# Kernel optimization log

Hardware: AMD Instinct MI355X
Metric: run time of the kernel (lower is better)

The kernel has to match this reference:

```python
import jax, jax.numpy as jnp
import numpy as np

B, N, L, H, V, OV, MAX_STEPS = 16, 256, 4, 128, 512, 1000, 48


def setup_inputs() -> dict:
    key = jax.random.key(0)
    ks = jax.random.split(key, 20)
    s = lambda fan_in: 1.0 / np.sqrt(fan_in)
    return {
        'data': jax.random.randint(ks[0], (B, N, L), 0, V, dtype=jnp.int32),
        'true_branch_nodes': jax.random.randint(ks[1], (B, N), 0, N, dtype=jnp.int32),
        'false_branch_nodes': jax.random.randint(ks[2], (B, N), 0, N, dtype=jnp.int32),
        'start_index': jax.random.randint(ks[3], (B,), 0, N, dtype=jnp.int32),
        'exit_index': jax.random.randint(ks[4], (B,), 0, N, dtype=jnp.int32),
        'steps': jax.random.randint(ks[5], (B,), 1, MAX_STEPS + 1, dtype=jnp.int32),
        'embed_w': jax.random.uniform(ks[6], (V, H), jnp.float32, -0.1, 0.1),
        'Wi0': jax.random.normal(ks[7], (H, 4 * H), jnp.float32) * s(H),
        'Wh0': jax.random.normal(ks[8], (H, 4 * H), jnp.float32) * s(H),
        'b0': jnp.zeros((4 * H,), jnp.float32),
        'Wi1': jax.random.normal(ks[9], (H, 4 * H), jnp.float32) * s(H),
        'Wh1': jax.random.normal(ks[10], (H, 4 * H), jnp.float32) * s(H),
        'b1': jnp.zeros((4 * H,), jnp.float32),
        'branch_w': jax.random.normal(ks[11], (4 * H, 2), jnp.float32) * s(4 * H),
        'branch_b': jax.random.normal(ks[12], (2,), jnp.float32) * 1e-6,
        'out_w': jax.random.normal(ks[13], (H, OV), jnp.float32) * s(H),
        'out_b': jax.random.normal(ks[14], (OV,), jnp.float32) * 1e-6,
    }


def _lstm(c, h, x, Wi, Wh, b):
    # flax LSTMCell gate order: i, f, g, o
    z = x @ Wi + h @ Wh + b
    i, f, g, o = jnp.split(z, 4, axis=-1)
    c = jax.nn.sigmoid(f) * c + jax.nn.sigmoid(i) * jnp.tanh(g)
    h = jax.nn.sigmoid(o) * jnp.tanh(c)
    return c, h


def reference(data, true_branch_nodes, false_branch_nodes, start_index, exit_index, steps,
              embed_w, Wi0, Wh0, b0, Wi1, Wh1, b1, branch_w, branch_b, out_w, out_b):
    num_nodes = data.shape[1]

    def single_example(data_e, true_idx, false_idx, start, exit_i, n_steps):
        emb_t = jnp.swapaxes(embed_w[data_e], 0, 1)  # [L, N, H]
        hs0 = tuple(jnp.zeros((num_nodes, H), embed_w.dtype) for _ in range(4))  # (c0,h0,c1,h1)
        ip0 = jnp.zeros((num_nodes,), embed_w.dtype).at[start].set(1.0)

        def execute(hs):
            # run 2-layer stacked LSTM over each node's statement tokens (vectorized over nodes)
            def tok_step(carry, x):
                c0, h0, c1, h1 = carry
                c0, h0 = _lstm(c0, h0, x, Wi0, Wh0, b0)
                c1, h1 = _lstm(c1, h1, h0, Wi1, Wh1, b1)
                return (c0, h0, c1, h1), None
            carry, _ = jax.lax.scan(tok_step, hs, emb_t)
            return carry

        def step(carry, idx):
            hs, ip = carry
            contrib = execute(hs)
            # exit node keeps its previous hidden state
            contrib = tuple(c.at[exit_i].set(h[exit_i]) for c, h in zip(contrib, hs))
            concat = jnp.concatenate(contrib, axis=-1)  # [N, 4H]
            p = jax.nn.softmax(concat @ branch_w + branch_b, axis=-1)
            pt, pf = p[:, 0], p[:, 1]
            wt, wf = pt * ip, pf * ip
            ip_new = (jax.ops.segment_sum(wt, true_idx, num_segments=num_nodes)
                      + jax.ops.segment_sum(wf, false_idx, num_segments=num_nodes))
            denom = (ip_new + 1e-7)[:, None]
            def agg(hleaf):
                t = jax.ops.segment_sum(hleaf * wt[:, None], true_idx, num_segments=num_nodes)
                f = jax.ops.segment_sum(hleaf * wf[:, None], false_idx, num_segments=num_nodes)
                return (t + f) / denom
            hs_new = tuple(agg(hleaf) for hleaf in contrib)
            active = idx < n_steps
            hs = tuple(jnp.where(active, new, old) for new, old in zip(hs_new, hs))
            ip = jnp.where(active, ip_new, ip)
            return (hs, ip), None

        (hs, ip), _ = jax.lax.scan(step, (hs0, ip0), jnp.arange(MAX_STEPS))
        return hs[3][exit_i] @ out_w + out_b  # top-layer h at exit node -> [OV]

    return jax.vmap(single_example)(data, true_branch_nodes, false_branch_nodes,
                                    start_index, exit_index, steps)
```

## Files before the change

kernel.cpp:

```cpp
#include <hip/hip_runtime.h>

namespace {
constexpr int B = 16, N = 256, L = 4, H = 128, V = 512, OV = 1000, MAX_STEPS = 48;
constexpr int Z = 4 * H;
constexpr int BN = B * N;
constexpr int PADK = 132;
}

typedef __attribute__((ext_vector_type(8))) short short8;
typedef __attribute__((ext_vector_type(4))) float f32x4;

union F8 {
    short8 s;
    uint4 u;
    uint2 h[2];
};

__device__ __forceinline__ float sigf(float x) { return 1.0f / (1.0f + __expf(-x)); }
__device__ __forceinline__ float tanh_f(float x) { return 1.0f - 2.0f / (__expf(2.0f * x) + 1.0f); }

__device__ __forceinline__ unsigned short bf16_rne(float x) {
    unsigned u = __float_as_uint(x);
    return (unsigned short)((u + 0x7fffu + ((u >> 16) & 1u)) >> 16);
}
__device__ __forceinline__ void split2(float x, unsigned short& hi, unsigned short& lo) {
    hi = bf16_rne(x);
    const float hf = __uint_as_float(((unsigned)hi) << 16);
    lo = bf16_rne(x - hf);
}

__global__ __launch_bounds__(256) void k_init(float4* __restrict__ cur4,
                                              float* __restrict__ ip,
                                              const int* __restrict__ start) {
    const int idx = blockIdx.x * 256 + threadIdx.x;
    cur4[idx] = make_float4(0.f, 0.f, 0.f, 0.f);
    if (idx < BN) ip[idx] = ((idx & (N - 1)) == start[idx >> 8]) ? 1.0f : 0.0f;
}

__global__ __launch_bounds__(256) void k_tokz(const float* __restrict__ emb,
                                              const float* __restrict__ Wi0,
                                              const float* __restrict__ b0,
                                              float* __restrict__ tokz) {
    __shared__ float lds_a[16 * 128];
    float4* l4 = (float4*)lds_a;
    const int tid = threadIdx.x;
    const int c = tid & 127, rg = tid >> 7;
    const int row0 = blockIdx.x * 16;
    {
        const float4* a4 = (const float4*)emb;
        l4[tid] = a4[row0 * 32 + tid];
        l4[tid + 256] = a4[row0 * 32 + tid + 256];
    }
    __syncthreads();
    float acc[8][4];
    {
        float bq[4];
#pragma unroll
        for (int q = 0; q < 4; q++) bq[q] = b0[c + q * 128];
#pragma unroll
        for (int i = 0; i < 8; i++)
#pragma unroll
            for (int q = 0; q < 4; q++) acc[i][q] = bq[q];
    }
    for (int k4 = 0; k4 < 32; k4++) {
        float4 a[8];
#pragma unroll
        for (int i = 0; i < 8; i++) a[i] = l4[(rg * 8 + i) * 32 + k4];
#pragma unroll
        for (int j = 0; j < 4; j++) {
            const int k = k4 * 4 + j;
            const float* wr = Wi0 + k * Z + c;
            const float w0 = wr[0], w1 = wr[128], w2 = wr[256], w3 = wr[384];
#pragma unroll
            for (int i = 0; i < 8; i++) {
                const float av = (j == 0) ? a[i].x : (j == 1) ? a[i].y : (j == 2) ? a[i].z : a[i].w;
                acc[i][0] += av * w0;
                acc[i][1] += av * w1;
                acc[i][2] += av * w2;
                acc[i][3] += av * w3;
            }
        }
    }
#pragma unroll
    for (int i = 0; i < 8; i++) {
        const int row = row0 + rg * 8 + i;
#pragma unroll
        for (int q = 0; q < 4; q++) tokz[row * Z + c + q * 128] = acc[i][q];
    }
}

__global__ __launch_bounds__(256) void k_pack(const float* __restrict__ Wh0,
                                              const float* __restrict__ Wi1,
                                              const float* __restrict__ Wh1,
                                              unsigned short* __restrict__ WPhi,
                                              unsigned short* __restrict__ WPlo) {
    const int gid = blockIdx.x * 256 + threadIdx.x;
    const int lp = gid & 63;
    const int ks = (gid >> 6) & 3;
    const int w = (gid >> 8) & 7;
    const int q = (gid >> 11) & 3;
    const int split = (gid >> 13) & 1;
    const int mat = gid >> 14;
    const float* W = (mat == 0) ? Wh0 : (mat == 1) ? Wi1 : Wh1;
    const int g = lp >> 4, li = lp & 15;
    const int col = q * 128 + w * 16 + li;
    const int e = ((mat * 4 + q) * 8 + w) * 4 + ks;
    unsigned short* dst = (split ? WPlo : WPhi) + (size_t)e * 512 + lp * 8;
#pragma unroll
    for (int j = 0; j < 8; j++) {
        const int k = ks * 32 + ((j & 4) ? 16 : 0) + g * 4 + (j & 3);
        const float x = W[k * Z + col];
        const unsigned short hi = bf16_rne(x);
        unsigned short v = hi;
        if (split) {
            const float hf = __uint_as_float(((unsigned)hi) << 16);
            v = bf16_rne(x - hf);
        }
        dst[j] = v;
    }
}

__global__ __launch_bounds__(256) void k_csr(const int* __restrict__ tix,
                                             const int* __restrict__ fix,
                                             int* __restrict__ off,
                                             int* __restrict__ ent) {
    const int b = blockIdx.x;
    const int m = threadIdx.x;
    __shared__ int cnt[N];
    __shared__ int wsum[4];
    cnt[m] = 0;
    __syncthreads();
    const int ti = tix[b * N + m];
    const int fi = fix[b * N + m];
    atomicAdd(&cnt[ti], 1);
    atomicAdd(&cnt[fi], 1);
    __syncthreads();
    const int v = cnt[m];
    const int lane = m & 63, w = m >> 6;
    int sc = v;
#pragma unroll
    for (int o = 1; o < 64; o <<= 1) {
        const int t = __shfl_up(sc, o);
        if (lane >= o) sc += t;
    }
    if (lane == 63) wsum[w] = sc;
    __syncthreads();
    int add = 0;
    for (int i = 0; i < w; i++) add += wsum[i];
    const int base = sc - v + add;
    off[b * (N + 1) + m] = base;
    if (m == N - 1) off[b * (N + 1) + N] = base + v;
    __syncthreads();
    cnt[m] = base;
    __syncthreads();
    const int p1 = atomicAdd(&cnt[ti], 1);
    ent[b * 2 * N + p1] = (m << 1);
    const int p2 = atomicAdd(&cnt[fi], 1);
    ent[b * 2 * N + p2] = (m << 1) | 1;
}

__global__ __launch_bounds__(512, 1) void k_scan(
    const float* __restrict__ c0c, const float* __restrict__ h0c,
    const float* __restrict__ c1c, const float* __restrict__ h1c,
    float* __restrict__ c0w, float* __restrict__ h0w,
    float* __restrict__ c1w, float* __restrict__ h1w,
    const unsigned short* __restrict__ WPhi, const unsigned short* __restrict__ WPlo,
    const float* __restrict__ b1,
    const float* __restrict__ tokz, const int* __restrict__ data,
    const float* __restrict__ bw, const float* __restrict__ bb,
    const float* __restrict__ ip, float* __restrict__ wt, float* __restrict__ wf,
    const int* __restrict__ exiti, const int* __restrict__ steps, const int s) {
    const int bx = blockIdx.x;
    const int b = bx >> 4;
    if (s >= steps[b]) return;
    const int row0 = bx * 16;
    const int tid = threadIdx.x;
    const int w = tid >> 6;
    const int l = tid & 63;
    const int g = l >> 4, li = l & 15;
    const int ch = w * 16 + li;

    __shared__ unsigned short h0hi[16 * PADK], h0lo[16 * PADK];
    __shared__ unsigned short h1hi[16 * PADK], h1lo[16 * PADK];
    __shared__ float red[16][8][2];

    float c0[4], c1[4], h0[4], h1[4];
#pragma unroll
    for (int r = 0; r < 4; r++) {
        const int off = (row0 + g * 4 + r) * H + ch;
        c0[r] = c0c[off];
        h0[r] = h0c[off];
        c1[r] = c1c[off];
        h1[r] = h1c[off];
    }
    float b1v[4];
#pragma unroll
    for (int q = 0; q < 4; q++) b1v[q] = b1[q * 128 + ch];

#pragma unroll
    for (int r = 0; r < 4; r++) {
        unsigned short hi, lo;
        split2(h0[r], hi, lo);
        h0hi[(g * 4 + r) * PADK + ch] = hi;
        h0lo[(g * 4 + r) * PADK + ch] = lo;
        split2(h1[r], hi, lo);
        h1hi[(g * 4 + r) * PADK + ch] = hi;
        h1lo[(g * 4 + r) * PADK + ch] = lo;
    }
    __syncthreads();

#pragma unroll 1
    for (int t = 0; t < L; t++) {
        f32x4 acc[4];
        {
            int tok[4];
#pragma unroll
            for (int r = 0; r < 4; r++) tok[r] = data[(row0 + g * 4 + r) * L + t];
#pragma unroll
            for (int q = 0; q < 4; q++)
#pragma unroll
                for (int r = 0; r < 4; r++) acc[q][r] = tokz[tok[r] * Z + q * 128 + ch];
        }
#pragma unroll
        for (int ks = 0; ks < 4; ks++) {
            F8 ahi, alo;
            const int ab = li * PADK + ks * 32 + g * 4;
            ahi.h[0] = *(const uint2*)&h0hi[ab];
            ahi.h[1] = *(const uint2*)&h0hi[ab + 16];
            alo.h[0] = *(const uint2*)&h0lo[ab];
            alo.h[1] = *(const uint2*)&h0lo[ab + 16];
#pragma unroll
            for (int q = 0; q < 4; q++) {
                F8 bhi, blo;
                const int e = ((0 * 4 + q) * 8 + w) * 4 + ks;
                bhi.u = *(const uint4*)(WPhi + (size_t)e * 512 + l * 8);
                blo.u = *(const uint4*)(WPlo + (size_t)e * 512 + l * 8);
                acc[q] = __builtin_amdgcn_mfma_f32_16x16x32_bf16(ahi.s, bhi.s, acc[q], 0, 0, 0);
                acc[q] = __builtin_amdgcn_mfma_f32_16x16x32_bf16(ahi.s, blo.s, acc[q], 0, 0, 0);
                acc[q] = __builtin_amdgcn_mfma_f32_16x16x32_bf16(alo.s, bhi.s, acc[q], 0, 0, 0);
            }
        }
#pragma unroll
        for (int r = 0; r < 4; r++) {
            const float cn = sigf(acc[1][r]) * c0[r] + sigf(acc[0][r]) * tanh_f(acc[2][r]);
            c0[r] = cn;
            h0[r] = sigf(acc[3][r]) * tanh_f(cn);
        }
        __syncthreads();
#pragma unroll
        for (int r = 0; r < 4; r++) {
            unsigned short hi, lo;
            split2(h0[r], hi, lo);
            h0hi[(g * 4 + r) * PADK + ch] = hi;
            h0lo[(g * 4 + r) * PADK + ch] = lo;
        }
        __syncthreads();
#pragma unroll
        for (int q = 0; q < 4; q++) {
            const float bv = b1v[q];
            acc[q][0] = bv; acc[q][1] = bv; acc[q][2] = bv; acc[q][3] = bv;
        }
#pragma unroll
        for (int ks = 0; ks < 4; ks++) {
            F8 a0hi, a0lo, a1hi, a1lo;
            const int ab = li * PADK + ks * 32 + g * 4;
            a0hi.h[0] = *(const uint2*)&h0hi[ab];
            a0hi.h[1] = *(const uint2*)&h0hi[ab + 16];
            a0lo.h[0] = *(const uint2*)&h0lo[ab];
            a0lo.h[1] = *(const uint2*)&h0lo[ab + 16];
            a1hi.h[0] = *(const uint2*)&h1hi[ab];
            a1hi.h[1] = *(const uint2*)&h1hi[ab + 16];
            a1lo.h[0] = *(const uint2*)&h1lo[ab];
            a1lo.h[1] = *(const uint2*)&h1lo[ab + 16];
#pragma unroll
            for (int q = 0; q < 4; q++) {
                F8 b1hi, b1lo, b2hi, b2lo;
                const int e1 = ((1 * 4 + q) * 8 + w) * 4 + ks;
                const int e2 = ((2 * 4 + q) * 8 + w) * 4 + ks;
                b1hi.u = *(const uint4*)(WPhi + (size_t)e1 * 512 + l * 8);
                b1lo.u = *(const uint4*)(WPlo + (size_t)e1 * 512 + l * 8);
                b2hi.u = *(const uint4*)(WPhi + (size_t)e2 * 512 + l * 8);
                b2lo.u = *(const uint4*)(WPlo + (size_t)e2 * 512 + l * 8);
                acc[q] = __builtin_amdgcn_mfma_f32_16x16x32_bf16(a0hi.s, b1hi.s, acc[q], 0, 0, 0);
                acc[q] = __builtin_amdgcn_mfma_f32_16x16x32_bf16(a0hi.s, b1lo.s, acc[q], 0, 0, 0);
                acc[q] = __builtin_amdgcn_mfma_f32_16x16x32_bf16(a0lo.s, b1hi.s, acc[q], 0, 0, 0);
                acc[q] = __builtin_amdgcn_mfma_f32_16x16x32_bf16(a1hi.s, b2hi.s, acc[q], 0, 0, 0);
                acc[q] = __builtin_amdgcn_mfma_f32_16x16x32_bf16(a1hi.s, b2lo.s, acc[q], 0, 0, 0);
                acc[q] = __builtin_amdgcn_mfma_f32_16x16x32_bf16(a1lo.s, b2hi.s, acc[q], 0, 0, 0);
            }
        }
#pragma unroll
        for (int r = 0; r < 4; r++) {
            const float cn = sigf(acc[1][r]) * c1[r] + sigf(acc[0][r]) * tanh_f(acc[2][r]);
            c1[r] = cn;
            h1[r] = sigf(acc[3][r]) * tanh_f(cn);
        }
        __syncthreads();
#pragma unroll
        for (int r = 0; r < 4; r++) {
            unsigned short hi, lo;
            split2(h1[r], hi, lo);
            h1hi[(g * 4 + r) * PADK + ch] = hi;
            h1lo[(g * 4 + r) * PADK + ch] = lo;
        }
        __syncthreads();
    }

    const int ex = exiti[b];
    if ((ex >> 4) == (bx & 15)) {
        const int rl = ex & 15;
#pragma unroll
        for (int r = 0; r < 4; r++) {
            if (g * 4 + r == rl) {
                const int off = (row0 + rl) * H + ch;
                c0[r] = c0c[off];
                h0[r] = h0c[off];
                c1[r] = c1c[off];
                h1[r] = h1c[off];
            }
        }
    }
#pragma unroll
    for (int r = 0; r < 4; r++) {
        const int off = (row0 + g * 4 + r) * H + ch;
        c0w[off] = c0[r];
        h0w[off] = h0[r];
        c1w[off] = c1[r];
        h1w[off] = h1[r];
    }
    float2 bwv[4];
#pragma unroll
    for (int x = 0; x < 4; x++) bwv[x] = ((const float2*)bw)[x * 128 + ch];
    float l0p[4], l1p[4];
#pragma unroll
    for (int r = 0; r < 4; r++) {
        l0p[r] = c0[r] * bwv[0].x + h0[r] * bwv[1].x + c1[r] * bwv[2].x + h1[r] * bwv[3].x;
        l1p[r] = c0[r] * bwv[0].y + h0[r] * bwv[1].y + c1[r] * bwv[2].y + h1[r] * bwv[3].y;
    }
#pragma unroll
    for (int off = 8; off > 0; off >>= 1)
#pragma unroll
        for (int r = 0; r < 4; r++) {
            l0p[r] += __shfl_xor(l0p[r], off);
            l1p[r] += __shfl_xor(l1p[r], off);
        }
    if (li == 0)
#pragma unroll
        for (int r = 0; r < 4; r++) {
            red[g * 4 + r][w][0] = l0p[r];
            red[g * 4 + r][w][1] = l1p[r];
        }
    __syncthreads();
    if (tid < 16) {
        float l0 = bb[0], l1 = bb[1];
#pragma unroll
        for (int ww = 0; ww < 8; ww++) {
            l0 += red[tid][ww][0];
            l1 += red[tid][ww][1];
        }
        const float m = fmaxf(l0, l1);
        const float e0 = __expf(l0 - m), e1 = __expf(l1 - m);
        const float inv = 1.0f / (e0 + e1);
        const float ipv = ip[row0 + tid];
        wt[row0 + tid] = e0 * inv * ipv;
        wf[row0 + tid] = e1 * inv * ipv;
    }
}

__global__ __launch_bounds__(256) void k_agg(
    const float* __restrict__ c0w, const float* __restrict__ h0w,
    const float* __restrict__ c1w, const float* __restrict__ h1w,
    float* __restrict__ c0c, float* __restrict__ h0c,
    float* __restrict__ c1c, float* __restrict__ h1c,
    const int* __restrict__ off, const int* __restrict__ ent,
    const float* __restrict__ wt, const float* __restrict__ wf,
    float* __restrict__ ip, const int* __restrict__ steps, const int s) {
    const int row00 = blockIdx.x * 4;
    const int b = row00 >> 8;
    if (s >= steps[b]) return;
    const int tid = threadIdx.x;
    const int lane = tid & 63;
    const int n = (row00 & (N - 1)) + (tid >> 6);
    const int rowb = b * N;
    const int beg = off[b * (N + 1) + n];
    const int end = off[b * (N + 1) + n + 1];
    float a00 = 0, a01 = 0, a10 = 0, a11 = 0, a20 = 0, a21 = 0, a30 = 0, a31 = 0;
    float ipacc = 0.f;
    for (int e = beg; e < end; e++) {
        const int pe = ent[b * 2 * N + e];
        const int m = pe >> 1;
        const float wgt = (pe & 1) ? wf[rowb + m] : wt[rowb + m];
        ipacc += wgt;
        const int rb = (rowb + m) * H;
        a00 += c0w[rb + lane] * wgt;
        a01 += c0w[rb + lane + 64] * wgt;
        a10 += h0w[rb + lane] * wgt;
        a11 += h0w[rb + lane + 64] * wgt;
        a20 += c1w[rb + lane] * wgt;
        a21 += c1w[rb + lane + 64] * wgt;
        a30 += h1w[rb + lane] * wgt;
        a31 += h1w[rb + lane + 64] * wgt;
    }
    const float dn = 1.0f / (ipacc + 1e-7f);
    const int ob = (rowb + n) * H;
    c0c[ob + lane] = a00 * dn;
    c0c[ob + lane + 64] = a01 * dn;
    h0c[ob + lane] = a10 * dn;
    h0c[ob + lane + 64] = a11 * dn;
    c1c[ob + lane] = a20 * dn;
    c1c[ob + lane + 64] = a21 * dn;
    h1c[ob + lane] = a30 * dn;
    h1c[ob + lane + 64] = a31 * dn;
    if (lane == 0) ip[rowb + n] = ipacc;
}

__global__ __launch_bounds__(256) void k_out(const float* __restrict__ h1c,
                                             const float* __restrict__ ow,
                                             const float* __restrict__ ob,
                                             const int* __restrict__ exiti,
                                             float* __restrict__ out) {
    const int b = blockIdx.x;
    __shared__ float h[H];
    const int tid = threadIdx.x;
    if (tid < H) h[tid] = h1c[(b * N + exiti[b]) * H + tid];
    __syncthreads();
    for (int v = tid; v < OV; v += 256) {
        float acc = ob[v];
        for (int d = 0; d < H; d++) acc += h[d] * ow[d * OV + v];
        out[b * OV + v] = acc;
    }
}

extern "C" void kernel_launch(void* const* d_in, const int* in_sizes, int n_in,
                              void* d_out, int out_size, void* d_ws, size_t ws_size,
                              hipStream_t stream) {
    (void)in_sizes; (void)n_in; (void)out_size;
    const int* data = (const int*)d_in[0];
    const int* tix = (const int*)d_in[1];
    const int* fix = (const int*)d_in[2];
    const int* start = (const int*)d_in[3];
    const int* exiti = (const int*)d_in[4];
    const int* steps = (const int*)d_in[5];
    const float* emb = (const float*)d_in[6];
    const float* Wi0 = (const float*)d_in[7];
    const float* Wh0 = (const float*)d_in[8];
    const float* b0 = (const float*)d_in[9];
    const float* Wi1 = (const float*)d_in[10];
    const float* Wh1 = (const float*)d_in[11];
    const float* b1 = (const float*)d_in[12];
    const float* bw = (const float*)d_in[13];
    const float* bb = (const float*)d_in[14];
    const float* ow = (const float*)d_in[15];
    const float* obias = (const float*)d_in[16];
    float* out = (float*)d_out;

    const size_t SB = (size_t)BN * H;
    float* ws = (float*)d_ws;
    float* c0c = ws;
    float* h0c = ws + 1 * SB;
    float* c1c = ws + 2 * SB;
    float* h1c = ws + 3 * SB;
    float* c0w = ws + 4 * SB;
    float* h0w = ws + 5 * SB;
    float* c1w = ws + 6 * SB;
    float* h1w = ws + 7 * SB;
    float* tokz = ws + 8 * SB;
    float* ip = tokz + (size_t)V * Z;
    float* wt = ip + BN;
    float* wf = wt + BN;
    unsigned short* WPhi = (unsigned short*)(wf + BN);
    unsigned short* WPlo = WPhi + 3 * 65536;
    int* csr_off = (int*)(WPlo + 3 * 65536);
    int* csr_ent = csr_off + B * (N + 1);
    const size_t need = (8 * SB + (size_t)V * Z + 3 * (size_t)BN) * sizeof(float) +
                        2 * 3 * 65536 * sizeof(unsigned short) +
                        (B * (N + 1) + B * 2 * N) * sizeof(int);
    if (ws_size < need) return;

    k_init<<<(4 * SB / 4) / 256, 256, 0, stream>>>((float4*)ws, ip, start);
    k_tokz<<<V / 16, 256, 0, stream>>>(emb, Wi0, b0, tokz);
    k_pack<<<192, 256, 0, stream>>>(Wh0, Wi1, Wh1, WPhi, WPlo);
    k_csr<<<B, 256, 0, stream>>>(tix, fix, csr_off, csr_ent);

    for (int s = 0; s < MAX_STEPS; s++) {
        k_scan<<<BN / 16, 512, 0, stream>>>(c0c, h0c, c1c, h1c, c0w, h0w, c1w, h1w,
                                            WPhi, WPlo, b1, tokz, data, bw, bb,
                                            ip, wt, wf, exiti, steps, s);
        k_agg<<<BN / 4, 256, 0, stream>>>(c0w, h0w, c1w, h1w, c0c, h0c, c1c, h1c,
                                          csr_off, csr_ent, wt, wf, ip, steps, s);
    }
    k_out<<<B, 256, 0, stream>>>(h1c, ow, obias, exiti, out);
}
```

Baseline: 4.774 ms.

## Fuse per-step scan/aggregate kernels into one persistent cooperative kernel with grid sync

Replaces the 96 per-step k_scan/k_agg launches, plus the init and output kernels, with a single cooperative persistent kernel. Each block keeps its 16 nodes' LSTM state in shared memory across steps. A grid.sync separates the LSTM/branch phase from the CSR aggregation, and the work buffers are double-buffered so the next step's writes cannot race the current step's reads. This removes launch overhead and the global round-trip of the current state, at the cost of grid-wide barriers and a requirement that all 256 blocks of 512 threads be co-resident.

New measurement: 7.522 ms. 57.6% more time.

```diff
diff --git a/kernel.cpp b/kernel.cpp
--- a/kernel.cpp
+++ b/kernel.cpp
@@ -1,10 +1,14 @@
 #include <hip/hip_runtime.h>
+#include <hip/hip_cooperative_groups.h>
+
+namespace cg = cooperative_groups;
 
 namespace {
 constexpr int B = 16, N = 256, L = 4, H = 128, V = 512, OV = 1000, MAX_STEPS = 48;
 constexpr int Z = 4 * H;
 constexpr int BN = B * N;
 constexpr int PADK = 132;
+constexpr int SB = BN * H;
 }
 
 typedef __attribute__((ext_vector_type(8))) short short8;
@@ -27,14 +31,6 @@
     hi = bf16_rne(x);
     const float hf = __uint_as_float(((unsigned)hi) << 16);
     lo = bf16_rne(x - hf);
-}
-
-__global__ __launch_bounds__(256) void k_init(float4* __restrict__ cur4,
-                                              float* __restrict__ ip,
-                                              const int* __restrict__ start) {
-    const int idx = blockIdx.x * 256 + threadIdx.x;
-    cur4[idx] = make_float4(0.f, 0.f, 0.f, 0.f);
-    if (idx < BN) ip[idx] = ((idx & (N - 1)) == start[idx >> 8]) ? 1.0f : 0.0f;
 }
 
 __global__ __launch_bounds__(256) void k_tokz(const float* __restrict__ emb,
@@ -159,275 +155,275 @@
     ent[b * 2 * N + p2] = (m << 1) | 1;
 }
 
-__global__ __launch_bounds__(512, 1) void k_scan(
-    const float* __restrict__ c0c, const float* __restrict__ h0c,
-    const float* __restrict__ c1c, const float* __restrict__ h1c,
-    float* __restrict__ c0w, float* __restrict__ h0w,
-    float* __restrict__ c1w, float* __restrict__ h1w,
+__global__ __launch_bounds__(512, 2) void k_persist(
     const unsigned short* __restrict__ WPhi, const unsigned short* __restrict__ WPlo,
-    const float* __restrict__ b1,
-    const float* __restrict__ tokz, const int* __restrict__ data,
-    const float* __restrict__ bw, const float* __restrict__ bb,
-    const float* __restrict__ ip, float* __restrict__ wt, float* __restrict__ wf,
-    const int* __restrict__ exiti, const int* __restrict__ steps, const int s) {
+    const float* __restrict__ b1, const float* __restrict__ tokz,
+    const int* __restrict__ data, const float* __restrict__ bw,
+    const float* __restrict__ bb,
+    float* __restrict__ work0, float* __restrict__ work1,
+    float* __restrict__ wtwf0, float* __restrict__ wtwf1,
+    const int* __restrict__ csr_off, const int* __restrict__ csr_ent,
+    const int* __restrict__ start, const int* __restrict__ exiti,
+    const int* __restrict__ steps, const float* __restrict__ ow,
+    const float* __restrict__ obias, float* __restrict__ h1fin,
+    float* __restrict__ out) {
     const int bx = blockIdx.x;
     const int b = bx >> 4;
-    if (s >= steps[b]) return;
+    const int nbase = (bx & 15) * 16;
     const int row0 = bx * 16;
     const int tid = threadIdx.x;
     const int w = tid >> 6;
     const int l = tid & 63;
     const int g = l >> 4, li = l & 15;
     const int ch = w * 16 + li;
-
+    cg::grid_group grid = cg::this_grid();
+
+    __shared__ float cur[4][16][132];
     __shared__ unsigned short h0hi[16 * PADK], h0lo[16 * PADK];
     __shared__ unsigned short h1hi[16 * PADK], h1lo[16 * PADK];
     __shared__ float red[16][8][2];
-
-    float c0[4], c1[4], h0[4], h1[4];
-#pragma unroll
-    for (int r = 0; r < 4; r++) {
-        const int off = (row0 + g * 4 + r) * H + ch;
-        c0[r] = c0c[off];
-        h0[r] = h0c[off];
-        c1[r] = c1c[off];
-        h1[r] = h1c[off];
-    }
+    __shared__ float ip_l[16];
+
+    const int mysteps = steps[b];
+    const int ex = exiti[b];
+    int rex = -1;
+    if ((ex >> 4) == (bx & 15) && ((ex & 15) >> 2) == g) rex = ex & 3;
+
+    for (int i = tid; i < 4 * 16 * 132; i += 512) ((float*)cur)[i] = 0.f;
+    if (tid < 16) ip_l[tid] = (nbase + tid == start[b]) ? 1.0f : 0.0f;
+
     float b1v[4];
 #pragma unroll
     for (int q = 0; q < 4; q++) b1v[q] = b1[q * 128 + ch];
-
-#pragma unroll
-    for (int r = 0; r < 4; r++) {
-        unsigned short hi, lo;
-        split2(h0[r], hi, lo);
-        h0hi[(g * 4 + r) * PADK + ch] = hi;
-        h0lo[(g * 4 + r) * PADK + ch] = lo;
-        split2(h1[r], hi, lo);
-        h1hi[(g * 4 + r) * PADK + ch] = hi;
-        h1lo[(g * 4 + r) * PADK + ch] = lo;
-    }
-    __syncthreads();
+    float2 bwv[4];
+#pragma unroll
+    for (int x = 0; x < 4; x++) bwv[x] = ((const float2*)bw)[x * 128 + ch];
+    const float bb0 = bb[0], bb1 = bb[1];
+    __syncthreads();
+
+    for (int s = 0; s < MAX_STEPS; s++) {
+        const bool active = (s < mysteps);
+        float* Wk = (s & 1) ? work1 : work0;
+        float* wtp = (s & 1) ? wtwf1 : wtwf0;
+        float* wfp = wtp + BN;
+
+        if (active) {
+            float c0[4], h0[4], c1[4], h1[4];
+#pragma unroll
+            for (int r = 0; r < 4; r++) {
+                const int rl = g * 4 + r;
+                c0[r] = cur[0][rl][ch];
+                h0[r] = cur[1][rl][ch];
+                c1[r] = cur[2][rl][ch];
+                h1[r] = cur[3][rl][ch];
+            }
+            float sc0 = 0, sh0 = 0, sc1 = 0, sh1 = 0;
+            if (rex >= 0) { sc0 = c0[rex]; sh0 = h0[rex]; sc1 = c1[rex]; sh1 = h1[rex]; }
+#pragma unroll
+            for (int r = 0; r < 4; r++) {
+                unsigned short hi, lo;
+                split2(h0[r], hi, lo);
+                h0hi[(g * 4 + r) * PADK + ch] = hi;
+                h0lo[(g * 4 + r) * PADK + ch] = lo;
+                split2(h1[r], hi, lo);
+                h1hi[(g * 4 + r) * PADK + ch] = hi;
+                h1lo[(g * 4 + r) * PADK + ch] = lo;
+            }
+            __syncthreads();
 
 #pragma unroll 1
-    for (int t = 0; t < L; t++) {
-        f32x4 acc[4];
-        {
-            int tok[4];
-#pragma unroll
-            for (int r = 0; r < 4; r++) tok[r] = data[(row0 + g * 4 + r) * L + t];
-#pragma unroll
-            for (int q = 0; q < 4; q++)
-#pragma unroll
-                for (int r = 0; r < 4; r++) acc[q][r] = tokz[tok[r] * Z + q * 128 + ch];
+            for (int t = 0; t < L; t++) {
+                f32x4 acc[4];
+                {
+                    int tok[4];
+#pragma unroll
+                    for (int r = 0; r < 4; r++) tok[r] = data[(row0 + g * 4 + r) * L + t];
+#pragma unroll
+                    for (int q = 0; q < 4; q++)
+#pragma unroll
+                        for (int r = 0; r < 4; r++) acc[q][r] = tokz[tok[r] * Z + q * 128 + ch];
+                }
+#pragma unroll
+                for (int ks = 0; ks < 4; ks++) {
+                    F8 ahi, alo;
+                    const int ab = li * PADK + ks * 32 + g * 4;
+                    ahi.h[0] = *(const uint2*)&h0hi[ab];
+                    ahi.h[1] = *(const uint2*)&h0hi[ab + 16];
+                    alo.h[0] = *(const uint2*)&h0lo[ab];
+                    alo.h[1] = *(const uint2*)&h0lo[ab + 16];
+#pragma unroll
+                    for (int q = 0; q < 4; q++) {
+                        F8 bhi, blo;
+                        const int e = ((0 * 4 + q) * 8 + w) * 4 + ks;
+                        bhi.u = *(const uint4*)(WPhi + (size_t)e * 512 + l * 8);
+                        blo.u = *(const uint4*)(WPlo + (size_t)e * 512 + l * 8);
+                        acc[q] = __builtin_amdgcn_mfma_f32_16x16x32_bf16(ahi.s, bhi.s, acc[q], 0, 0, 0);
+                        acc[q] = __builtin_amdgcn_mfma_f32_16x16x32_bf16(ahi.s, blo.s, acc[q], 0, 0, 0);
+                        acc[q] = __builtin_amdgcn_mfma_f32_16x16x32_bf16(alo.s, bhi.s, acc[q], 0, 0, 0);
+                    }
+                }
+#pragma unroll
+                for (int r = 0; r < 4; r++) {
+                    const float cn = sigf(acc[1][r]) * c0[r] + sigf(acc[0][r]) * tanh_f(acc[2][r]);
+                    c0[r] = cn;
+                    h0[r] = sigf(acc[3][r]) * tanh_f(cn);
+                }
+                __syncthreads();
+#pragma unroll
+                for (int r = 0; r < 4; r++) {
+                    unsigned short hi, lo;
+                    split2(h0[r], hi, lo);
+                    h0hi[(g * 4 + r) * PADK + ch] = hi;
+                    h0lo[(g * 4 + r) * PADK + ch] = lo;
+                }
+                __syncthreads();
+#pragma unroll
+                for (int q = 0; q < 4; q++) {
+                    const float bv = b1v[q];
+                    acc[q][0] = bv; acc[q][1] = bv; acc[q][2] = bv; acc[q][3] = bv;
+                }
+#pragma unroll
+                for (int ks = 0; ks < 4; ks++) {
+                    F8 a0hi, a0lo, a1hi, a1lo;
+                    const int ab = li * PADK + ks * 32 + g * 4;
+                    a0hi.h[0] = *(const uint2*)&h0hi[ab];
+                    a0hi.h[1] = *(const uint2*)&h0hi[ab + 16];
+                    a0lo.h[0] = *(const uint2*)&h0lo[ab];
+                    a0lo.h[1] = *(const uint2*)&h0lo[ab + 16];
+                    a1hi.h[0] = *(const uint2*)&h1hi[ab];
+                    a1hi.h[1] = *(const uint2*)&h1hi[ab + 16];
+                    a1lo.h[0] = *(const uint2*)&h1lo[ab];
+                    a1lo.h[1] = *(const uint2*)&h1lo[ab + 16];
+#pragma unroll
+                    for (int q = 0; q < 4; q++) {
+                        F8 b1hi, b1lo, b2hi, b2lo;
+                        const int e1 = ((1 * 4 + q) * 8 + w) * 4 + ks;
+                        const int e2 = ((2 * 4 + q) * 8 + w) * 4 + ks;
+                        b1hi.u = *(const uint4*)(WPhi + (size_t)e1 * 512 + l * 8);
+                        b1lo.u = *(const uint4*)(WPlo + (size_t)e1 * 512 + l * 8);
+                        b2hi.u = *(const uint4*)(WPhi + (size_t)e2 * 512 + l * 8);
+                        b2lo.u = *(const uint4*)(WPlo + (size_t)e2 * 512 + l * 8);
+                        acc[q] = __builtin_amdgcn_mfma_f32_16x16x32_bf16(a0hi.s, b1hi.s, acc[q], 0, 0, 0);
+                        acc[q] = __builtin_amdgcn_mfma_f32_16x16x32_bf16(a0hi.s, b1lo.s, acc[q], 0, 0, 0);
+                        acc[q] = __builtin_amdgcn_mfma_f32_16x16x32_bf16(a0lo.s, b1hi.s, acc[q], 0, 0, 0);
+                        acc[q] = __builtin_amdgcn_mfma_f32_16x16x32_bf16(a1hi.s, b2hi.s, acc[q], 0, 0, 0);
+                        acc[q] = __builtin_amdgcn_mfma_f32_16x16x32_bf16(a1hi.s, b2lo.s, acc[q], 0, 0, 0);
+                        acc[q] = __builtin_amdgcn_mfma_f32_16x16x32_bf16(a1lo.s, b2hi.s, acc[q], 0, 0, 0);
+                    }
+                }
+#pragma unroll
+                for (int r = 0; r < 4; r++) {
+                    const float cn = sigf(acc[1][r]) * c1[r] + sigf(acc[0][r]) * tanh_f(acc[2][r]);
+                    c1[r] = cn;
+                    h1[r] = sigf(acc[3][r]) * tanh_f(cn);
+                }
+                __syncthreads();
+#pragma unroll
+                for (int r = 0; r < 4; r++) {
+                    unsigned short hi, lo;
+                    split2(h1[r], hi, lo);
+                    h1hi[(g * 4 + r) * PADK + ch] = hi;
+                    h1lo[(g * 4 + r) * PADK + ch] = lo;
+                }
+                __syncthreads();
+            }
+
+            if (rex >= 0) { c0[rex] = sc0; h0[rex] = sh0; c1[rex] = sc1; h1[rex] = sh1; }
+#pragma unroll
+            for (int r = 0; r < 4; r++) {
+                const int off = (row0 + g * 4 + r) * H + ch;
+                Wk[off] = c0[r];
+                Wk[SB + off] = h0[r];
+                Wk[2 * SB + off] = c1[r];
+                Wk[3 * SB + off] = h1[r];
+            }
+            float l0p[4], l1p[4];
+#pragma unroll
+            for (int r = 0; r < 4; r++) {
+                l0p[r] = c0[r] * bwv[0].x + h0[r] * bwv[1].x + c1[r] * bwv[2].x + h1[r] * bwv[3].x;
+                l1p[r] = c0[r] * bwv[0].y + h0[r] * bwv[1].y + c1[r] * bwv[2].y + h1[r] * bwv[3].y;
+            }
+#pragma unroll
+            for (int off = 8; off > 0; off >>= 1)
+#pragma unroll
+                for (int r = 0; r < 4; r++) {
+                    l0p[r] += __shfl_xor(l0p[r], off);
+                    l1p[r] += __shfl_xor(l1p[r], off);
+                }
+            if (li == 0)
+#pragma unroll
+                for (int r = 0; r < 4; r++) {
+                    red[g * 4 + r][w][0] = l0p[r];
+                    red[g * 4 + r][w][1] = l1p[r];
+                }
+            __syncthreads();
+            if (tid < 16) {
+                float l0 = bb0, l1 = bb1;
+#pragma unroll
+                for (int ww = 0; ww < 8; ww++) {
+                    l0 += red[tid][ww][0];
+                    l1 += red[tid][ww][1];
+                }
+                const float m = fmaxf(l0, l1);
+                const float e0 = __expf(l0 - m), e1 = __expf(l1 - m);
+                const float inv = 1.0f / (e0 + e1);
+                const float ipv = ip_l[tid];
+                wtp[row0 + tid] = e0 * inv * ipv;
+                wfp[row0 + tid] = e1 * inv * ipv;
+            }
         }
-#pragma unroll
-        for (int ks = 0; ks < 4; ks++) {
-            F8 ahi, alo;
-            const int ab = li * PADK + ks * 32 + g * 4;
-            ahi.h[0] = *(const uint2*)&h0hi[ab];
-            ahi.h[1] = *(const uint2*)&h0hi[ab + 16];
-            alo.h[0] = *(const uint2*)&h0lo[ab];
-            alo.h[1] = *(const uint2*)&h0lo[ab + 16];
-#pragma unroll
-            for (int q = 0; q < 4; q++) {
-                F8 bhi, blo;
-                const int e = ((0 * 4 + q) * 8 + w) * 4 + ks;
-                bhi.u = *(const uint4*)(WPhi + (size_t)e * 512 + l * 8);
-                blo.u = *(const uint4*)(WPlo + (size_t)e * 512 + l * 8);
-                acc[q] = __builtin_amdgcn_mfma_f32_16x16x32_bf16(ahi.s, bhi.s, acc[q], 0, 0, 0);
-                acc[q] = __builtin_amdgcn_mfma_f32_16x16x32_bf16(ahi.s, blo.s, acc[q], 0, 0, 0);
-                acc[q] = __builtin_amdgcn_mfma_f32_16x16x32_bf16(alo.s, bhi.s, acc[q], 0, 0, 0);
-            }
-        }
-#pragma unroll
-        for (int r = 0; r < 4; r++) {
-            const float cn = sigf(acc[1][r]) * c0[r] + sigf(acc[0][r]) * tanh_f(acc[2][r]);
-            c0[r] = cn;
-            h0[r] = sigf(acc[3][r]) * tanh_f(cn);
+
+        grid.sync();
+
+        if (active) {
+            const int lane = l;
+#pragma unroll 1
+            for (int rr = 0; rr < 2; rr++) {
+                const int nloc = w * 2 + rr;
+                const int n = nbase + nloc;
+                const int beg = csr_off[b * (N + 1) + n];
+                const int end = csr_off[b * (N + 1) + n + 1];
+                float a00 = 0, a01 = 0, a10 = 0, a11 = 0, a20 = 0, a21 = 0, a30 = 0, a31 = 0;
+                float ipacc = 0.f;
+                for (int e = beg; e < end; e++) {
+                    const int pe = csr_ent[b * 2 * N + e];
+                    const int m = pe >> 1;
+                    const float wgt = (pe & 1) ? wfp[b * N + m] : wtp[b * N + m];
+                    ipacc += wgt;
+                    const int rb = (b * N + m) * H;
+                    a00 += Wk[rb + lane] * wgt;
+                    a01 += Wk[rb + lane + 64] * wgt;
+                    a10 += Wk[SB + rb + lane] * wgt;
+                    a11 += Wk[SB + rb + lane + 64] * wgt;
+                    a20 += Wk[2 * SB + rb + lane] * wgt;
+                    a21 += Wk[2 * SB + rb + lane + 64] * wgt;
+                    a30 += Wk[3 * SB + rb + lane] * wgt;
+                    a31 += Wk[3 * SB + rb + lane + 64] * wgt;
+                }
+                const float dn = 1.0f / (ipacc + 1e-7f);
+                cur[0][nloc][lane] = a00 * dn;
+                cur[0][nloc][lane + 64] = a01 * dn;
+                cur[1][nloc][lane] = a10 * dn;
+                cur[1][nloc][lane + 64] = a11 * dn;
+                cur[2][nloc][lane] = a20 * dn;
+                cur[2][nloc][lane + 64] = a21 * dn;
+                cur[3][nloc][lane] = a30 * dn;
+                cur[3][nloc][lane + 64] = a31 * dn;
+                if (lane == 0) ip_l[nloc] = ipacc;
+            }
         }
         __syncthreads();
-#pragma unroll
-        for (int r = 0; r < 4; r++) {
-            unsigned short hi, lo;
-            split2(h0[r], hi, lo);
-            h0hi[(g * 4 + r) * PADK + ch] = hi;
-            h0lo[(g * 4 + r) * PADK + ch] = lo;
+    }
+
+    if ((ex >> 4) == (bx & 15) && tid < 128) h1fin[b * H + tid] = cur[3][ex & 15][tid];
+    grid.sync();
+    if (bx < B) {
+        const int bb_ = bx;
+        for (int v = tid; v < OV; v += 512) {
+            float acc = obias[v];
+            for (int d = 0; d < H; d++) acc += h1fin[bb_ * H + d] * ow[d * OV + v];
+            out[bb_ * OV + v] = acc;
         }
-        __syncthreads();
-#pragma unroll
-        for (int q = 0; q < 4; q++) {
-            const float bv = b1v[q];
-            acc[q][0] = bv; acc[q][1] = bv; acc[q][2] = bv; acc[q][3] = bv;
-        }
-#pragma unroll
-        for (int ks = 0; ks < 4; ks++) {
-            F8 a0hi, a0lo, a1hi, a1lo;
-            const int ab = li * PADK + ks * 32 + g * 4;
-            a0hi.h[0] = *(const uint2*)&h0hi[ab];
-            a0hi.h[1] = *(const uint2*)&h0hi[ab + 16];
-            a0lo.h[0] = *(const uint2*)&h0lo[ab];
-            a0lo.h[1] = *(const uint2*)&h0lo[ab + 16];
-            a1hi.h[0] = *(const uint2*)&h1hi[ab];
-            a1hi.h[1] = *(const uint2*)&h1hi[ab + 16];
-            a1lo.h[0] = *(const uint2*)&h1lo[ab];
-            a1lo.h[1] = *(const uint2*)&h1lo[ab + 16];
-#pragma unroll
-            for (int q = 0; q < 4; q++) {
-                F8 b1hi, b1lo, b2hi, b2lo;
-                const int e1 = ((1 * 4 + q) * 8 + w) * 4 + ks;
-                const int e2 = ((2 * 4 + q) * 8 + w) * 4 + ks;
-                b1hi.u = *(const uint4*)(WPhi + (size_t)e1 * 512 + l * 8);
-                b1lo.u = *(const uint4*)(WPlo + (size_t)e1 * 512 + l * 8);
-                b2hi.u = *(const uint4*)(WPhi + (size_t)e2 * 512 + l * 8);
-                b2lo.u = *(const uint4*)(WPlo + (size_t)e2 * 512 + l * 8);
-                acc[q] = __builtin_amdgcn_mfma_f32_16x16x32_bf16(a0hi.s, b1hi.s, acc[q], 0, 0, 0);
-                acc[q] = __builtin_amdgcn_mfma_f32_16x16x32_bf16(a0hi.s, b1lo.s, acc[q], 0, 0, 0);
-                acc[q] = __builtin_amdgcn_mfma_f32_16x16x32_bf16(a0lo.s, b1hi.s, acc[q], 0, 0, 0);
-                acc[q] = __builtin_amdgcn_mfma_f32_16x16x32_bf16(a1hi.s, b2hi.s, acc[q], 0, 0, 0);
-                acc[q] = __builtin_amdgcn_mfma_f32_16x16x32_bf16(a1hi.s, b2lo.s, acc[q], 0, 0, 0);
-                acc[q] = __builtin_amdgcn_mfma_f32_16x16x32_bf16(a1lo.s, b2hi.s, acc[q], 0, 0, 0);
-            }
-        }
-#pragma unroll
-        for (int r = 0; r < 4; r++) {
-            const float cn = sigf(acc[1][r]) * c1[r] + sigf(acc[0][r]) * tanh_f(acc[2][r]);
-            c1[r] = cn;
-            h1[r] = sigf(acc[3][r]) * tanh_f(cn);
-        }
-        __syncthreads();
-#pragma unroll
-        for (int r = 0; r < 4; r++) {
-            unsigned short hi, lo;
-            split2(h1[r], hi, lo);
-            h1hi[(g * 4 + r) * PADK + ch] = hi;
-            h1lo[(g * 4 + r) * PADK + ch] = lo;
-        }
-        __syncthreads();
-    }
-
-    const int ex = exiti[b];
-    if ((ex >> 4) == (bx & 15)) {
-        const int rl = ex & 15;
-#pragma unroll
-        for (int r = 0; r < 4; r++) {
-            if (g * 4 + r == rl) {
-                const int off = (row0 + rl) * H + ch;
-                c0[r] = c0c[off];
-                h0[r] = h0c[off];
-                c1[r] = c1c[off];
-                h1[r] = h1c[off];
-            }
-        }
-    }
-#pragma unroll
-    for (int r = 0; r < 4; r++) {
-        const int off = (row0 + g * 4 + r) * H + ch;
-        c0w[off] = c0[r];
-        h0w[off] = h0[r];
-        c1w[off] = c1[r];
-        h1w[off] = h1[r];
-    }
-    float2 bwv[4];
-#pragma unroll
-    for (int x = 0; x < 4; x++) bwv[x] = ((const float2*)bw)[x * 128 + ch];
-    float l0p[4], l1p[4];
-#pragma unroll
-    for (int r = 0; r < 4; r++) {
-        l0p[r] = c0[r] * bwv[0].x + h0[r] * bwv[1].x + c1[r] * bwv[2].x + h1[r] * bwv[3].x;
-        l1p[r] = c0[r] * bwv[0].y + h0[r] * bwv[1].y + c1[r] * bwv[2].y + h1[r] * bwv[3].y;
-    }
-#pragma unroll
-    for (int off = 8; off > 0; off >>= 1)
-#pragma unroll
-        for (int r = 0; r < 4; r++) {
-            l0p[r] += __shfl_xor(l0p[r], off);
-            l1p[r] += __shfl_xor(l1p[r], off);
-        }
-    if (li == 0)
-#pragma unroll
-        for (int r = 0; r < 4; r++) {
-            red[g * 4 + r][w][0] = l0p[r];
-            red[g * 4 + r][w][1] = l1p[r];
-        }
-    __syncthreads();
-    if (tid < 16) {
-        float l0 = bb[0], l1 = bb[1];
-#pragma unroll
-        for (int ww = 0; ww < 8; ww++) {
-            l0 += red[tid][ww][0];
-            l1 += red[tid][ww][1];
-        }
-        const float m = fmaxf(l0, l1);
-        const float e0 = __expf(l0 - m), e1 = __expf(l1 - m);
-        const float inv = 1.0f / (e0 + e1);
-        const float ipv = ip[row0 + tid];
-        wt[row0 + tid] = e0 * inv * ipv;
-        wf[row0 + tid] = e1 * inv * ipv;
-    }
-}
-
-__global__ __launch_bounds__(256) void k_agg(
-    const float* __restrict__ c0w, const float* __restrict__ h0w,
-    const float* __restrict__ c1w, const float* __restrict__ h1w,
-    float* __restrict__ c0c, float* __restrict__ h0c,
-    float* __restrict__ c1c, float* __restrict__ h1c,
-    const int* __restrict__ off, const int* __restrict__ ent,
-    const float* __restrict__ wt, const float* __restrict__ wf,
-    float* __restrict__ ip, const int* __restrict__ steps, const int s) {
-    const int row00 = blockIdx.x * 4;
-    const int b = row00 >> 8;
-    if (s >= steps[b]) return;
-    const int tid = threadIdx.x;
-    const int lane = tid & 63;
-    const int n = (row00 & (N - 1)) + (tid >> 6);
-    const int rowb = b * N;
-    const int beg = off[b * (N + 1) + n];
-    const int end = off[b * (N + 1) + n + 1];
-    float a00 = 0, a01 = 0, a10 = 0, a11 = 0, a20 = 0, a21 = 0, a30 = 0, a31 = 0;
-    float ipacc = 0.f;
-    for (int e = beg; e < end; e++) {
-        const int pe = ent[b * 2 * N + e];
-        const int m = pe >> 1;
-        const float wgt = (pe & 1) ? wf[rowb + m] : wt[rowb + m];
-        ipacc += wgt;
-        const int rb = (rowb + m) * H;
-        a00 += c0w[rb + lane] * wgt;
-        a01 += c0w[rb + lane + 64] * wgt;
-        a10 += h0w[rb + lane] * wgt;
-        a11 += h0w[rb + lane + 64] * wgt;
-        a20 += c1w[rb + lane] * wgt;
-        a21 += c1w[rb + lane + 64] * wgt;
-        a30 += h1w[rb + lane] * wgt;
-        a31 += h1w[rb + lane + 64] * wgt;
-    }
-    const float dn = 1.0f / (ipacc + 1e-7f);
-    const int ob = (rowb + n) * H;
-    c0c[ob + lane] = a00 * dn;
-    c0c[ob + lane + 64] = a01 * dn;
-    h0c[ob + lane] = a10 * dn;
-    h0c[ob + lane + 64] = a11 * dn;
-    c1c[ob + lane] = a20 * dn;
-    c1c[ob + lane + 64] = a21 * dn;
-    h1c[ob + lane] = a30 * dn;
-    h1c[ob + lane + 64] = a31 * dn;
-    if (lane == 0) ip[rowb + n] = ipacc;
-}
-
-__global__ __launch_bounds__(256) void k_out(const float* __restrict__ h1c,
-                                             const float* __restrict__ ow,
-                                             const float* __restrict__ ob,
-                                             const int* __restrict__ exiti,
-                                             float* __restrict__ out) {
-    const int b = blockIdx.x;
-    __shared__ float h[H];
-    const int tid = threadIdx.x;
-    if (tid < H) h[tid] = h1c[(b * N + exiti[b]) * H + tid];
-    __syncthreads();
-    for (int v = tid; v < OV; v += 256) {
-        float acc = ob[v];
-        for (int d = 0; d < H; d++) acc += h[d] * ow[d * OV + v];
-        out[b * OV + v] = acc;
     }
 }
 
@@ -443,8 +439,8 @@
     const int* steps = (const int*)d_in[5];
     const float* emb = (const float*)d_in[6];
     const float* Wi0 = (const float*)d_in[7];
+    const float* b0 = (const float*)d_in[9];
     const float* Wh0 = (const float*)d_in[8];
-    const float* b0 = (const float*)d_in[9];
     const float* Wi1 = (const float*)d_in[10];
     const float* Wh1 = (const float*)d_in[11];
     const float* b1 = (const float*)d_in[12];
@@ -454,40 +450,31 @@
     const float* obias = (const float*)d_in[16];
     float* out = (float*)d_out;
 
-    const size_t SB = (size_t)BN * H;
     float* ws = (float*)d_ws;
-    float* c0c = ws;
-    float* h0c = ws + 1 * SB;
-    float* c1c = ws + 2 * SB;
-    float* h1c = ws + 3 * SB;
-    float* c0w = ws + 4 * SB;
-    float* h0w = ws + 5 * SB;
-    float* c1w = ws + 6 * SB;
-    float* h1w = ws + 7 * SB;
-    float* tokz = ws + 8 * SB;
-    float* ip = tokz + (size_t)V * Z;
-    float* wt = ip + BN;
-    float* wf = wt + BN;
-    unsigned short* WPhi = (unsigned short*)(wf + BN);
+    float* tokz = ws;
+    float* work0 = tokz + (size_t)V * Z;
+    float* work1 = work0 + 4 * (size_t)SB;
+    float* wtwf0 = work1 + 4 * (size_t)SB;
+    float* wtwf1 = wtwf0 + 2 * BN;
+    float* h1fin = wtwf1 + 2 * BN;
+    unsigned short* WPhi = (unsigned short*)(h1fin + B * H);
     unsigned short* WPlo = WPhi + 3 * 65536;
     int* csr_off = (int*)(WPlo + 3 * 65536);
     int* csr_ent = csr_off + B * (N + 1);
-    const size_t need = (8 * SB + (size_t)V * Z + 3 * (size_t)BN) * sizeof(float) +
-                        2 * 3 * 65536 * sizeof(unsigned short) +
-                        (B * (N + 1) + B * 2 * N) * sizeof(int);
+    const size_t need = ((size_t)V * Z + 8 * (size_t)SB + 4 * BN + B * H) * 4 +
+                        6 * 65536 * 2 + (B * (N + 1) + 2 * B * N) * 4;
     if (ws_size < need) return;
 
-    k_init<<<(4 * SB / 4) / 256, 256, 0, stream>>>((float4*)ws, ip, start);
     k_tokz<<<V / 16, 256, 0, stream>>>(emb, Wi0, b0, tokz);
     k_pack<<<192, 256, 0, stream>>>(Wh0, Wi1, Wh1, WPhi, WPlo);
     k_csr<<<B, 256, 0, stream>>>(tix, fix, csr_off, csr_ent);
 
-    for (int s = 0; s < MAX_STEPS; s++) {
-        k_scan<<<BN / 16, 512, 0, stream>>>(c0c, h0c, c1c, h1c, c0w, h0w, c1w, h1w,
-                                            WPhi, WPlo, b1, tokz, data, bw, bb,
-                                            ip, wt, wf, exiti, steps, s);
-        k_agg<<<BN / 4, 256, 0, stream>>>(c0w, h0w, c1w, h1w, c0c, h0c, c1c, h1c,
-                                          csr_off, csr_ent, wt, wf, ip, steps, s);
-    }
-    k_out<<<B, 256, 0, stream>>>(h1c, ow, obias, exiti, out);
-}
+    void* args[] = {(void*)&WPhi, (void*)&WPlo, (void*)&b1, (void*)&tokz,
+                    (void*)&data, (void*)&bw, (void*)&bb,
+                    (void*)&work0, (void*)&work1, (void*)&wtwf0, (void*)&wtwf1,
+                    (void*)&csr_off, (void*)&csr_ent,
+                    (void*)&start, (void*)&exiti, (void*)&steps,
+                    (void*)&ow, (void*)&obias, (void*)&h1fin, (void*)&out};
+    hipLaunchCooperativeKernel((const void*)k_persist, dim3(BN / 16), dim3(512),
+                               args, 0, stream);
+}
```
